# Kernel optimization log

Hardware: AMD Instinct MI355X
Metric: run time of the kernel (lower is better)

Reference implementation:

```python
import jax, jax.numpy as jnp
import numpy as np

ALPHA = 0.1        # axis_aligned_projection threshold
NEG_INF = -1e30    # large negative used for masking (softmax-equivalent to -inf)


def axis_aligned_projection(x, alpha=ALPHA):
    x_abs = jnp.abs(x)
    max_vals = jnp.max(x_abs, axis=-1, keepdims=True)
    axis_weights = jnp.where(x_abs >= alpha * max_vals, x_abs, 0.0)
    return axis_weights * jnp.sign(x)


def setup_inputs() -> dict:
    key = jax.random.key(0)
    kq, kk, kv = jax.random.split(key, 3)
    B, L, H, E = 4, 2048, 8, 64
    S, D = L, E
    queries = jax.random.normal(kq, (B, L, H, E), dtype=jnp.float32)
    keys = jax.random.normal(kk, (B, S, H, E), dtype=jnp.float32)
    values = jax.random.normal(kv, (B, S, H, D), dtype=jnp.float32)
    # TriangularCausalMask: True strictly above the diagonal -> masked out
    causal = jnp.triu(jnp.ones((L, S), dtype=jnp.bool_), k=1)
    attn_mask = jnp.broadcast_to(causal[None, None], (B, 1, L, S))
    return {"queries": queries, "keys": keys, "values": values, "attn_mask": attn_mask}


def reference(queries, keys, values, attn_mask):
    B, L, H, E = queries.shape
    scale = 1.0 / jnp.sqrt(jnp.float32(E))
    q = axis_aligned_projection(queries)
    k = axis_aligned_projection(keys)
    # [B,H,L,S] dense scores (the module materializes the full matrix)
    scores = jnp.einsum('blhe,bshe->bhls', q, k)
    scores = jnp.where(attn_mask, NEG_INF, scores)
    A = jax.nn.softmax(scale * scores, axis=-1)  # dropout is identity in eval mode
    V = jnp.einsum('bhls,bshd->blhd', A, values)
    return V
```

## Files before the change

### kernel.cpp

```cpp
#include <hip/hip_runtime.h>
#include <hip/hip_bf16.h>
#include <stdint.h>

#define B_ 4
#define L_ 2048
#define H_ 8
#define E_ 64
#define ALPHA 0.1f
#define LOG2E 1.44269504088896f
#define QSCALE (0.125f * LOG2E)
#define KSTR 72

typedef float f32x4 __attribute__((ext_vector_type(4)));
typedef short bf16x8 __attribute__((ext_vector_type(8)));
typedef short bf16x4 __attribute__((ext_vector_type(4)));
typedef uint32_t u32;
typedef unsigned short u16;
typedef u32 u32x2 __attribute__((ext_vector_type(2)));

__device__ __forceinline__ u16 f2bf(float f) {
    u32 x = __builtin_bit_cast(u32, f);
    u32 r = x + 0x7fffu + ((x >> 16) & 1u);
    return (u16)(r >> 16);
}

__device__ __forceinline__ u32 pk2bf(float a, float b) {
    u32 ua = __builtin_bit_cast(u32, a) + 0x8000u;
    u32 ub = __builtin_bit_cast(u32, b) + 0x8000u;
    return (ua >> 16) | (ub & 0xffff0000u);
}

__device__ __forceinline__ f32x4 mfma16x16x16bf16(bf16x4 a, bf16x4 b, f32x4 c) {
#if __has_builtin(__builtin_amdgcn_mfma_f32_16x16x16bf16_1k)
    return __builtin_amdgcn_mfma_f32_16x16x16bf16_1k(a, b, c, 0, 0, 0);
#elif __has_builtin(__builtin_amdgcn_mfma_f32_16x16x16_bf16)
    return __builtin_amdgcn_mfma_f32_16x16x16_bf16(a, b, c, 0, 0, 0);
#else
    f32x4 d;
    asm volatile("v_mfma_f32_16x16x16_bf16 %0, %1, %2, %3"
                 : "=v"(d) : "v"(a), "v"(b), "v"(c));
    return d;
#endif
}

__device__ __forceinline__ void dma16(const u16* g, u16* l) {
    __builtin_amdgcn_global_load_lds(
        (const __attribute__((address_space(1))) void*)g,
        (__attribute__((address_space(3))) void*)l, 16, 0, 0);
}

__global__ __launch_bounds__(256) void prep_kernel(const float* __restrict__ qin,
                                                   const float* __restrict__ kin,
                                                   const float* __restrict__ vin,
                                                   u16* __restrict__ qp,
                                                   u16* __restrict__ kp,
                                                   u16* __restrict__ vt) {
    __shared__ u16 tile[64][66];
    if (blockIdx.x < 4096) {
        const int RG = (B_ * L_ * H_) / 8;
        int wave = threadIdx.x >> 6, lane = threadIdx.x & 63;
        int g = blockIdx.x * 4 + wave;
        const float* src;
        u16* dst;
        int gr, ostr;
        float sc;
        if (g < RG) { src = qin; dst = qp; gr = g; sc = QSCALE; ostr = 64; }
        else        { src = kin; dst = kp; gr = g - RG; sc = 1.0f; ostr = KSTR; }

        int rig = lane >> 3;
        int c = (lane & 7) * 4;
        int row = gr * 8 + rig;

        const float* rp = src + (size_t)row * 64;
        float4 v0 = *(const float4*)(rp + c);
        float4 v1 = *(const float4*)(rp + c + 32);
        float f[8] = {v0.x, v0.y, v0.z, v0.w, v1.x, v1.y, v1.z, v1.w};

        float mx = 0.f;
#pragma unroll
        for (int i = 0; i < 8; ++i) mx = fmaxf(mx, fabsf(f[i]));
#pragma unroll
        for (int m = 1; m < 8; m <<= 1) mx = fmaxf(mx, __shfl_xor(mx, m));
        float thr = ALPHA * mx;

        u16 o[8];
#pragma unroll
        for (int i = 0; i < 8; ++i)
            o[i] = (fabsf(f[i]) >= thr) ? f2bf(f[i] * sc) : (u16)0;

        int b = row >> 14;
        int l = (row >> 3) & (L_ - 1);
        int h = row & 7;
        u16* orow = dst + ((size_t)(b * H_ + h) * L_ + l) * ostr;
        uint2 p0 = {(u32)o[0] | ((u32)o[1] << 16), (u32)o[2] | ((u32)o[3] << 16)};
        uint2 p1 = {(u32)o[4] | ((u32)o[5] << 16), (u32)o[6] | ((u32)o[7] << 16)};
        *(uint2*)(orow + c) = p0;
        *(uint2*)(orow + c + 32) = p1;
    } else {
        int bx = blockIdx.x - 4096;
        int bh = bx >> 5, sblk = bx & 31;
        int b = bh >> 3, h = bh & 7;
        int t = threadIdx.x;
        int s0 = sblk * 64;

#pragma unroll
        for (int p = 0; p < 2; ++p) {
            int sl = p * 32 + (t >> 3);
            int c = (t & 7) * 4;
            const float* rp = vin + (((size_t)(b * L_ + s0 + sl)) * H_ + h) * 64;
            float4 a = *(const float4*)(rp + c);
            float4 bb = *(const float4*)(rp + c + 32);
            u32* d0 = (u32*)&tile[sl][c];
            d0[0] = (u32)f2bf(a.x) | ((u32)f2bf(a.y) << 16);
            d0[1] = (u32)f2bf(a.z) | ((u32)f2bf(a.w) << 16);
            u32* d1 = (u32*)&tile[sl][c + 32];
            d1[0] = (u32)f2bf(bb.x) | ((u32)f2bf(bb.y) << 16);
            d1[1] = (u32)f2bf(bb.z) | ((u32)f2bf(bb.w) << 16);
        }
        __syncthreads();
#pragma unroll
        for (int p = 0; p < 2; ++p) {
            int d = p * 32 + (t >> 3);
            int sc2 = (t & 7) * 8;
            u16 o[8];
#pragma unroll
            for (int i = 0; i < 8; ++i) o[i] = tile[sc2 + i][d];
            uint4 val;
            val.x = (u32)o[0] | ((u32)o[1] << 16);
            val.y = (u32)o[2] | ((u32)o[3] << 16);
            val.z = (u32)o[4] | ((u32)o[5] << 16);
            val.w = (u32)o[6] | ((u32)o[7] << 16);
            *(uint4*)(vt + ((size_t)(bh * 32 + sblk) * 64 + d) * KSTR + sc2) = val;
        }
    }
}

__global__ __launch_bounds__(256, 4) void flash_kernel(const u16* __restrict__ Qp,
                                                       const u16* __restrict__ Kp,
                                                       const u16* __restrict__ Vt,
                                                       float* __restrict__ out) {
    __shared__ u16 kbuf[2][64 * KSTR];
    __shared__ u16 vbuf[2][64 * KSTR];
    int t = threadIdx.x;
    int wave = t >> 6, lane = t & 63;
    int bh = blockIdx.x & 31;
    int r5 = blockIdx.x >> 5;
    int g = r5 & 7, kr = r5 >> 3;
    int qq = (kr == 0) ? (31 - g) : (kr == 1) ? (16 + g) : (kr == 2) ? (15 - g) : g;
    int lo = lane & 15, quad = lane >> 4;
    int q0 = qq * 64 + wave * 16;
    int b = bh >> 3, h = bh & 7;

    const u16* kTiles = Kp + (size_t)bh * L_ * KSTR;
    const u16* vTiles = Vt + (size_t)bh * 32 * 64 * KSTR;

    auto stage = [&](int sb, int buf) {
        const u16* kg = kTiles + (size_t)sb * KSTR;
        const u16* vg = vTiles + (size_t)(sb >> 6) * 64 * KSTR;
        u16* kl = kbuf[buf];
        u16* vl = vbuf[buf];
        for (int i = wave; i < 18; i += 4) {
            if (i < 9) dma16(kg + i * 512 + lane * 8, kl + i * 512);
            else       dma16(vg + (i - 9) * 512 + lane * 8, vl + (i - 9) * 512);
        }
    };

    const u16* qbase = Qp + ((size_t)bh * L_ + q0 + lo) * 64 + quad * 8;
    bf16x8 aQ0 = *(const bf16x8*)(qbase);
    bf16x8 aQ1 = *(const bf16x8*)(qbase + 32);

    f32x4 o[4];
#pragma unroll
    for (int ni = 0; ni < 4; ++ni) o[ni] = (f32x4){0.f, 0.f, 0.f, 0.f};
    float ls = 0.f;

    auto frag_proc = [&](const u16* ks, const u16* vs, int sub, bool diag) {
        bf16x8 k0 = *(const bf16x8*)(ks + (sub * 16 + lo) * KSTR + quad * 8);
        bf16x8 k1 = *(const bf16x8*)(ks + (sub * 16 + lo) * KSTR + 32 + quad * 8);
        f32x4 S = {0.f, 0.f, 0.f, 0.f};
        S = __builtin_amdgcn_mfma_f32_16x16x32_bf16(k0, aQ0, S, 0, 0, 0);
        S = __builtin_amdgcn_mfma_f32_16x16x32_bf16(k1, aQ1, S, 0, 0, 0);

        bf16x4 vf[4];
#pragma unroll
        for (int ni = 0; ni < 4; ++ni)
            vf[ni] = *(const bf16x4*)(vs + (ni * 16 + lo) * KSTR + sub * 16 + quad * 4);

        float P[4];
#pragma unroll
        for (int r = 0; r < 4; ++r) {
            float e = __builtin_amdgcn_exp2f(S[r]);
            P[r] = (diag && (quad * 4 + r > lo)) ? 0.f : e;
        }
        ls += (P[0] + P[1]) + (P[2] + P[3]);
        u32x2 pk = {pk2bf(P[0], P[1]), pk2bf(P[2], P[3])};
        bf16x4 aP = __builtin_bit_cast(bf16x4, pk);
#pragma unroll
        for (int ni = 0; ni < 4; ++ni)
            o[ni] = mfma16x16x16bf16(aP, vf[ni], o[ni]);
    };

    stage(0, 0);
    __syncthreads();

    for (int kt = 0; kt < qq; ++kt) {
        int cur = kt & 1;
        stage((kt + 1) << 6, cur ^ 1);
        const u16* ks = kbuf[cur];
        const u16* vs = vbuf[cur];
#pragma unroll
        for (int sub = 0; sub < 4; ++sub) frag_proc(ks, vs, sub, false);
        __syncthreads();
    }

    {
        int cur = qq & 1;
        const u16* ks = kbuf[cur];
        const u16* vs = vbuf[cur];
        for (int sub = 0; sub < wave; ++sub) frag_proc(ks, vs, sub, false);
        frag_proc(ks, vs, wave, true);
    }

    ls += __shfl_xor(ls, 16);
    ls += __shfl_xor(ls, 32);
#pragma unroll
    for (int r = 0; r < 4; ++r) {
        float lr = __shfl(ls, quad * 4 + r);
        float inv = 1.0f / lr;
        int q = q0 + quad * 4 + r;
        float* ob = out + (((size_t)(b * L_ + q)) * H_ + h) * 64 + lo;
        ob[0]  = o[0][r] * inv;
        ob[16] = o[1][r] * inv;
        ob[32] = o[2][r] * inv;
        ob[48] = o[3][r] * inv;
    }
}

extern "C" void kernel_launch(void* const* d_in, const int* in_sizes, int n_in,
                              void* d_out, int out_size, void* d_ws, size_t ws_size,
                              hipStream_t stream) {
    const float* q = (const float*)d_in[0];
    const float* k = (const float*)d_in[1];
    const float* v = (const float*)d_in[2];
    float* out = (float*)d_out;

    const size_t QSZ = (size_t)B_ * H_ * L_ * 64;
    const size_t KSZ = (size_t)B_ * H_ * L_ * KSTR;
    u16* qp = (u16*)d_ws;
    u16* kp = qp + QSZ;
    u16* vt = kp + KSZ;

    prep_kernel<<<5120, 256, 0, stream>>>(q, k, v, qp, kp, vt);
    flash_kernel<<<1024, 256, 0, stream>>>(qp, kp, vt, out);
}
```

Before: 168.3 us.

## Split long causal query rows across two blocks and combine partial results

Each of the upper 16 query tiles now has its key range split into two blocks, for 1536 blocks instead of 1024 with shorter, more uniform work per block. Split blocks write unnormalized partial outputs and row sums to workspace, and a new combine kernel adds the two halves and normalizes. This targets the tail imbalance where the longest causal rows dominate runtime. The cost is an extra kernel launch and additional global traffic for the partial buffers. It also relies on exp2 without max subtraction, so the partials can be summed directly.

```diff
diff --git a/kernel.cpp b/kernel.cpp
--- a/kernel.cpp
+++ b/kernel.cpp
@@ -138,25 +138,37 @@
 __global__ __launch_bounds__(256, 4) void flash_kernel(const u16* __restrict__ Qp,
                                                        const u16* __restrict__ Kp,
                                                        const u16* __restrict__ Vt,
-                                                       float* __restrict__ out) {
+                                                       float* __restrict__ out,
+                                                       float* __restrict__ pO,
+                                                       float* __restrict__ pL) {
     __shared__ u16 kbuf[2][64 * KSTR];
     __shared__ u16 vbuf[2][64 * KSTR];
     int t = threadIdx.x;
     int wave = t >> 6, lane = t & 63;
     int bh = blockIdx.x & 31;
-    int r5 = blockIdx.x >> 5;
-    int g = r5 & 7, kr = r5 >> 3;
-    int qq = (kr == 0) ? (31 - g) : (kr == 1) ? (16 + g) : (kr == 2) ? (15 - g) : g;
+    int o5 = blockIdx.x >> 5;
     int lo = lane & 15, quad = lane >> 4;
-    int q0 = qq * 64 + wave * 16;
     int b = bh >> 3, h = bh & 7;
+
+    int group, t0, t1, slot;
+    bool diag;
+    if (o5 < 16)       { group = 16 + o5; t0 = 0;  t1 = 15;    diag = false; slot = 0; }
+    else if (o5 == 16) { group = 31;      t0 = 16; t1 = 31;    diag = true;  slot = 1; }
+    else if (o5 == 17) { group = 15;      t0 = 0;  t1 = 15;    diag = true;  slot = -1; }
+    else {
+        int op = o5 - 18;
+        int lam = 15 - (op >> 1);
+        if (!(op & 1)) { group = 15 + lam; t0 = 16; t1 = 15 + lam; diag = true; slot = 1; }
+        else           { group = lam - 1;  t0 = 0;  t1 = lam - 1;  diag = true; slot = -1; }
+    }
+    int q0 = group * 64 + wave * 16;
 
     const u16* kTiles = Kp + (size_t)bh * L_ * KSTR;
     const u16* vTiles = Vt + (size_t)bh * 32 * 64 * KSTR;
 
-    auto stage = [&](int sb, int buf) {
-        const u16* kg = kTiles + (size_t)sb * KSTR;
-        const u16* vg = vTiles + (size_t)(sb >> 6) * 64 * KSTR;
+    auto stage = [&](int tile, int buf) {
+        const u16* kg = kTiles + (size_t)tile * 64 * KSTR;
+        const u16* vg = vTiles + (size_t)tile * 64 * KSTR;
         u16* kl = kbuf[buf];
         u16* vl = vbuf[buf];
         for (int i = wave; i < 18; i += 4) {
@@ -174,7 +186,7 @@
     for (int ni = 0; ni < 4; ++ni) o[ni] = (f32x4){0.f, 0.f, 0.f, 0.f};
     float ls = 0.f;
 
-    auto frag_proc = [&](const u16* ks, const u16* vs, int sub, bool diag) {
+    auto frag_proc = [&](const u16* ks, const u16* vs, int sub, bool dg) {
         bf16x8 k0 = *(const bf16x8*)(ks + (sub * 16 + lo) * KSTR + quad * 8);
         bf16x8 k1 = *(const bf16x8*)(ks + (sub * 16 + lo) * KSTR + 32 + quad * 8);
         f32x4 S = {0.f, 0.f, 0.f, 0.f};
@@ -190,7 +202,7 @@
 #pragma unroll
         for (int r = 0; r < 4; ++r) {
             float e = __builtin_amdgcn_exp2f(S[r]);
-            P[r] = (diag && (quad * 4 + r > lo)) ? 0.f : e;
+            P[r] = (dg && (quad * 4 + r > lo)) ? 0.f : e;
         }
         ls += (P[0] + P[1]) + (P[2] + P[3]);
         u32x2 pk = {pk2bf(P[0], P[1]), pk2bf(P[2], P[3])};
@@ -200,12 +212,12 @@
             o[ni] = mfma16x16x16bf16(aP, vf[ni], o[ni]);
     };
 
-    stage(0, 0);
+    stage(t0, 0);
     __syncthreads();
 
-    for (int kt = 0; kt < qq; ++kt) {
-        int cur = kt & 1;
-        stage((kt + 1) << 6, cur ^ 1);
+    for (int kt = t0; kt < t1; ++kt) {
+        int cur = (kt - t0) & 1;
+        stage(kt + 1, cur ^ 1);
         const u16* ks = kbuf[cur];
         const u16* vs = vbuf[cur];
 #pragma unroll
@@ -214,25 +226,70 @@
     }
 
     {
-        int cur = qq & 1;
+        int cur = (t1 - t0) & 1;
         const u16* ks = kbuf[cur];
         const u16* vs = vbuf[cur];
-        for (int sub = 0; sub < wave; ++sub) frag_proc(ks, vs, sub, false);
-        frag_proc(ks, vs, wave, true);
+        if (diag) {
+            for (int sub = 0; sub < wave; ++sub) frag_proc(ks, vs, sub, false);
+            frag_proc(ks, vs, wave, true);
+        } else {
+#pragma unroll
+            for (int sub = 0; sub < 4; ++sub) frag_proc(ks, vs, sub, false);
+        }
     }
 
     ls += __shfl_xor(ls, 16);
     ls += __shfl_xor(ls, 32);
-#pragma unroll
-    for (int r = 0; r < 4; ++r) {
-        float lr = __shfl(ls, quad * 4 + r);
-        float inv = 1.0f / lr;
-        int q = q0 + quad * 4 + r;
-        float* ob = out + (((size_t)(b * L_ + q)) * H_ + h) * 64 + lo;
-        ob[0]  = o[0][r] * inv;
-        ob[16] = o[1][r] * inv;
-        ob[32] = o[2][r] * inv;
-        ob[48] = o[3][r] * inv;
+    if (slot < 0) {
+#pragma unroll
+        for (int r = 0; r < 4; ++r) {
+            float lr = __shfl(ls, quad * 4 + r);
+            float inv = 1.0f / lr;
+            int q = q0 + quad * 4 + r;
+            float* ob = out + (((size_t)(b * L_ + q)) * H_ + h) * 64 + lo;
+            ob[0]  = o[0][r] * inv;
+            ob[16] = o[1][r] * inv;
+            ob[32] = o[2][r] * inv;
+            ob[48] = o[3][r] * inv;
+        }
+    } else {
+        int gi = group - 16;
+        size_t sbase = ((size_t)(bh * 16 + gi) * 2 + slot);
+        float* po = pO + sbase * 4096 + (wave * 16 + quad * 4) * 64 + lo;
+#pragma unroll
+        for (int r = 0; r < 4; ++r) {
+            po[r * 64 + 0]  = o[0][r];
+            po[r * 64 + 16] = o[1][r];
+            po[r * 64 + 32] = o[2][r];
+            po[r * 64 + 48] = o[3][r];
+        }
+        if (quad == 0) pL[sbase * 64 + wave * 16 + lo] = ls;
+    }
+}
+
+__global__ __launch_bounds__(256) void combine_kernel(const float* __restrict__ pO,
+                                                      const float* __restrict__ pL,
+                                                      float* __restrict__ out) {
+    __shared__ float linv[64];
+    int bh = blockIdx.x & 31, gi = blockIdx.x >> 5;
+    int b = bh >> 3, h = bh & 7;
+    int group = 16 + gi;
+    int t = threadIdx.x;
+    size_t sb = (size_t)(bh * 16 + gi) * 2;
+    if (t < 64) linv[t] = 1.0f / (pL[sb * 64 + t] + pL[(sb + 1) * 64 + t]);
+    __syncthreads();
+    const float4* O1 = (const float4*)(pO + sb * 4096);
+    const float4* O2 = (const float4*)(pO + (sb + 1) * 4096);
+#pragma unroll
+    for (int k = 0; k < 4; ++k) {
+        int f4 = t * 4 + k;
+        int f = f4 * 4;
+        int ql = f >> 6, d = f & 63;
+        float4 a = O1[f4], c = O2[f4];
+        float s = linv[ql];
+        float4 r = {(a.x + c.x) * s, (a.y + c.y) * s, (a.z + c.z) * s, (a.w + c.w) * s};
+        int q = group * 64 + ql;
+        *(float4*)(out + (((size_t)(b * L_ + q)) * H_ + h) * 64 + d) = r;
     }
 }
 
@@ -249,7 +306,10 @@
     u16* qp = (u16*)d_ws;
     u16* kp = qp + QSZ;
     u16* vt = kp + KSZ;
+    float* pO = (float*)(vt + KSZ);
+    float* pL = pO + (size_t)32 * 16 * 2 * 4096;
 
     prep_kernel<<<5120, 256, 0, stream>>>(q, k, v, qp, kp, vt);
-    flash_kernel<<<1024, 256, 0, stream>>>(qp, kp, vt, out);
-}
+    flash_kernel<<<1536, 256, 0, stream>>>(qp, kp, vt, out, pO, pL);
+    combine_kernel<<<512, 256, 0, stream>>>(pO, pL, out);
+}
```

Measured after the change: 173.9 us. 3.3% more time.
